# Optimization experiments

Hardware: AMD Instinct MI355X
Metric: run time of the kernel (lower is better)

## Reference

```python
import jax, jax.numpy as jnp
import numpy as np

# PGA G(3,0,1), basis order [1, e0,e1,e2,e3, e01,e02,e03,e12,e13,e23, e012,e013,e023,e123, e0123].
# Non-degenerate blades (no e0 factor) kept by the inner-product mask:
INNER_COORDS = jnp.array([0, 2, 3, 4, 8, 9, 10, 14])

B, S, C_IN, MV = 4, 2048, 3, 16
HID, NH, BLADES = 32, 8, 9


def setup_inputs() -> dict:
    key = jax.random.key(0)
    ks = jax.random.split(key, 8)
    return {
        "x": jax.random.normal(ks[0], (B, S, C_IN, MV), dtype=jnp.float32),
        "blade": jax.random.normal(ks[1], (BLADES, MV, MV), dtype=jnp.float32) * 0.3,
        "w_enter": jax.random.uniform(ks[2], (HID, C_IN, BLADES), dtype=jnp.float32),
        "w_q": jax.random.uniform(ks[3], (HID * NH, HID, BLADES), dtype=jnp.float32),
        "w_k": jax.random.uniform(ks[4], (HID, HID, BLADES), dtype=jnp.float32),
        "w_v": jax.random.uniform(ks[5], (HID, HID, BLADES), dtype=jnp.float32),
        "w_out": jax.random.uniform(ks[6], (HID, HID * NH, BLADES), dtype=jnp.float32),
        "w_final": jax.random.uniform(ks[7], (HID, HID, BLADES), dtype=jnp.float32),
    }


def equi_linear(w, blade, x):
    # torch: einsum('j i b, b x y, ... i x -> ... j y'); fuse blade into weight first.
    wb = jnp.einsum("jib,bxy->jixy", w, blade)  # [out, in, 16, 16]
    return jnp.einsum("jixy,bsix->bsjy", wb, x)


def equi_norm(x):
    ip = jnp.sum(jnp.take(x, INNER_COORDS, axis=-1) ** 2, axis=-1, keepdims=True)
    sq = jnp.mean(ip, axis=-2, keepdims=True)  # mean over mv channels
    return x / jnp.sqrt(sq)


def geometric_attention(hn, blade, w_q, w_k, w_v, w_out):
    b, s = hn.shape[0], hn.shape[1]
    q = equi_linear(w_q, blade, hn)  # [b, s, HID*NH, 16]
    k = equi_linear(w_k, blade, hn)  # [b, s, HID, 16]
    v = equi_linear(w_v, blade, hn)
    # rearrange '... items (hidden n_heads) mv -> ... n_heads items hidden mv'
    q = q.reshape(b, s, HID, NH, MV).transpose(0, 3, 1, 2, 4)  # [b, nh, s, HID, 16]
    qs = jnp.take(q, INNER_COORDS, axis=-1).reshape(b, NH, s, HID * 8)
    ks = jnp.take(k, INNER_COORDS, axis=-1).reshape(b, s, HID * 8)  # shared head (dim 1)
    vs = v.reshape(b, s, HID * MV)
    scale = 1.0 / jnp.sqrt(jnp.asarray(HID * 8, dtype=qs.dtype))
    scores = jnp.einsum("bhsd,btd->bhst", qs, ks) * scale  # [b, nh, s, s]
    attn = jax.nn.softmax(scores, axis=-1)
    out = jnp.einsum("bhst,btd->bhsd", attn, vs)  # [b, nh, s, HID*16]
    out = out[..., : HID * MV].reshape(b, NH, s, HID, MV)
    # '... heads items hidden x -> ... items (heads hidden) x'
    out = out.transpose(0, 2, 1, 3, 4).reshape(b, s, NH * HID, MV)
    return equi_linear(w_out, blade, out)  # [b, s, HID, 16]


def reference(x, blade, w_enter, w_q, w_k, w_v, w_out, w_final):
    h = equi_linear(w_enter, blade, x)  # initial projection -> [b, s, HID, 16]
    res = h
    hn = equi_norm(h)  # attention_equinorm
    a = geometric_attention(hn, blade, w_q, w_k, w_v, w_out)
    h = res + a  # residual around attention block
    return equi_linear(w_final, blade, h)  # final output projection
```

## Files before the change

kernel.cpp:

```cpp
#include <hip/hip_runtime.h>


typedef unsigned short u16;
typedef unsigned int u32;
typedef __attribute__((ext_vector_type(4))) float f32x4;
typedef __attribute__((ext_vector_type(8))) _Float16 half8;

__device__ inline u16 f2h(float f) {
  _Float16 h = (_Float16)f;
  return __builtin_bit_cast(u16, h);
}
__device__ inline float h2f(u16 u) { return (float)__builtin_bit_cast(_Float16, u); }

__device__ inline void async_cp16(const void* g, void* l) {
  __builtin_amdgcn_global_load_lds((const __attribute__((address_space(1))) u32*)g,
                                   (__attribute__((address_space(3))) u32*)l, 16, 0, 0);
}

__device__ inline f32x4 mfma16(half8 a, half8 b, f32x4 c) {
  return __builtin_amdgcn_mfma_f32_16x16x32_f16(a, b, c, 0, 0, 0);
}

template <int CTRL>
__device__ inline float dpp_mv(float v) {
  int i = __builtin_bit_cast(int, v);
  return __builtin_bit_cast(float, __builtin_amdgcn_update_dpp(i, i, CTRL, 0xf, 0xf, false));
}

#define IC_PACK 0xEA984320u

#define Q_LD 4096

__global__ void build_wb_enter(const float* __restrict__ we, const float* __restrict__ blade,
                               float* __restrict__ out) {
  int idx = blockIdx.x * 256 + threadIdx.x;
  if (idx >= 32 * 48 * 16) return;
  int j = idx / 768;
  int rem = idx - j * 768;
  int ix = rem >> 4, y = rem & 15;
  int i = ix >> 4, x = ix & 15;
  float acc = 0.f;
#pragma unroll
  for (int bb = 0; bb < 9; ++bb) acc += we[j * 27 + i * 9 + bb] * blade[bb * 256 + x * 16 + y];
  out[idx] = acc;
}

__global__ void build_wqkvT(const float* __restrict__ wq, const float* __restrict__ wk,
                            const float* __restrict__ wv, const float* __restrict__ blade,
                            u16* __restrict__ out) {
  int idx = blockIdx.x * 256 + threadIdx.x;
  if (idx >= 2816 * 1024) return;
  int k = idx & 1023, n = idx >> 10;
  int kk = k & 511;
  int i = kk >> 4, x = kk & 15;
  const float* w;
  int y;
  float scale = 1.0f;
  if (n < 2048) {
    int j = n >> 3;
    y = (IC_PACK >> ((n & 7) * 4)) & 15;
    w = wq + j * 288 + i * 9;
    scale = 0.09016844005556021f;
  } else if (n < 2304) {
    int m = n - 2048;
    int j = m >> 3;
    y = (IC_PACK >> ((m & 7) * 4)) & 15;
    w = wk + j * 288 + i * 9;
  } else {
    int m = n - 2304;
    int j = m >> 4;
    y = m & 15;
    w = wv + j * 288 + i * 9;
  }
  float acc = 0.f;
#pragma unroll
  for (int bb = 0; bb < 9; ++bb) acc += w[bb] * blade[bb * 256 + x * 16 + y];
  out[idx] = f2h(acc * scale);
}

__global__ void build_woutT(const float* __restrict__ wo, const float* __restrict__ blade,
                            u16* __restrict__ out) {
  int idx = blockIdx.x * 256 + threadIdx.x;
  if (idx >= 512 * 4096) return;
  int k = idx & 4095, n = idx >> 12;
  int j = n >> 4, y = n & 15;
  int c = k >> 4, x = k & 15;
  float acc = 0.f;
#pragma unroll
  for (int bb = 0; bb < 9; ++bb) acc += wo[j * 2304 + c * 9 + bb] * blade[bb * 256 + x * 16 + y];
  out[idx] = f2h(acc);
}

__global__ void build_wfinalT(const float* __restrict__ wf, const float* __restrict__ blade,
                              u16* __restrict__ out) {
  int idx = blockIdx.x * 256 + threadIdx.x;
  if (idx >= 512 * 512) return;
  int k = idx & 511, n = idx >> 9;
  int j = n >> 4, y = n & 15;
  int i = k >> 4, x = k & 15;
  float acc = 0.f;
#pragma unroll
  for (int bb = 0; bb < 9; ++bb) acc += wf[j * 288 + i * 9 + bb] * blade[bb * 256 + x * 16 + y];
  out[idx] = f2h(acc);
}

__global__ __launch_bounds__(256) void enter_norm(const float* __restrict__ x,
                                                  const float* __restrict__ wb,
                                                  float* __restrict__ h, u16* __restrict__ hn) {
  const int tid = threadIdx.x;
  const int tl = tid >> 5, j = tid & 31;
  const int token = blockIdx.x * 8 + tl;
  const float* xp = x + (size_t)token * 48;
  float xv[48];
#pragma unroll
  for (int q = 0; q < 12; ++q) {
    float4 t = ((const float4*)xp)[q];
    xv[q * 4 + 0] = t.x;
    xv[q * 4 + 1] = t.y;
    xv[q * 4 + 2] = t.z;
    xv[q * 4 + 3] = t.w;
  }
  float acc[16] = {};
  const float* wp = wb + j * 768;
#pragma unroll
  for (int t = 0; t < 48; ++t) {
    const float xs = xv[t];
    const float4* w4 = (const float4*)(wp + t * 16);
#pragma unroll
    for (int u = 0; u < 4; ++u) {
      float4 wv = w4[u];
      acc[u * 4 + 0] += xs * wv.x;
      acc[u * 4 + 1] += xs * wv.y;
      acc[u * 4 + 2] += xs * wv.z;
      acc[u * 4 + 3] += xs * wv.w;
    }
  }
  float ip = acc[0] * acc[0] + acc[2] * acc[2] + acc[3] * acc[3] + acc[4] * acc[4] +
             acc[8] * acc[8] + acc[9] * acc[9] + acc[10] * acc[10] + acc[14] * acc[14];
#pragma unroll
  for (int d = 1; d < 32; d <<= 1) ip += __shfl_xor(ip, d, 64);
  const float r = 1.0f / sqrtf(ip * (1.0f / 32.0f));
  float* hp = h + (size_t)token * 512 + j * 16;
#pragma unroll
  for (int u = 0; u < 4; ++u)
    ((float4*)hp)[u] = make_float4(acc[u * 4 + 0], acc[u * 4 + 1], acc[u * 4 + 2], acc[u * 4 + 3]);
  u16 hb[16], lb[16];
#pragma unroll
  for (int y = 0; y < 16; ++y) {
    float sv = acc[y] * r;
    u16 hv = f2h(sv);
    hb[y] = hv;
    lb[y] = f2h(sv - h2f(hv));
  }
  u16* hq = hn + (size_t)token * 1024 + j * 16;
  ((uint4*)hq)[0] = *(const uint4*)&hb[0];
  ((uint4*)hq)[1] = *(const uint4*)&hb[8];
  u16* lq = hq + 512;
  ((uint4*)lq)[0] = *(const uint4*)&lb[0];
  ((uint4*)lq)[1] = *(const uint4*)&lb[8];
}

template <int MODE>
__global__ __launch_bounds__(256) void gemm_bt(const u16* __restrict__ A,
                                               const u16* __restrict__ BT, int M, int N, int K,
                                               u16* __restrict__ Co, float* __restrict__ Cf,
                                               const float* __restrict__ res,
                                               u16* __restrict__ kvp, int ldc) {
  __shared__ u16 ltA[4096];
  __shared__ u16 ltB[4096];
  const int tid = threadIdx.x;
  const int lane = tid & 63;
  const int wid = tid >> 6;
  const int quad = lane >> 4, colc = lane & 15;
  const int m0 = blockIdx.y * 128, n0 = blockIdx.x * 128;
  const int wrow = (wid >> 1) * 64, wcol = (wid & 1) * 64;
  f32x4 acc[4][4] = {};
  const int r0 = tid >> 2;
  const int swk = (((tid & 3) ^ ((tid >> 2) & 3)) << 3);
  const u16* Ab = A + (size_t)(m0 + r0) * K + swk;
  const u16* Ab2 = Ab + (size_t)64 * K;
  const u16* Bb = BT + (size_t)(n0 + r0) * K + swk;
  const u16* Bb2 = Bb + (size_t)64 * K;
  const int swr = ((colc & 3) << 3);
  for (int k0 = 0; k0 < K; k0 += 32) {
    __syncthreads();
    async_cp16(Ab + k0, &ltA[tid * 8]);
    async_cp16(Ab2 + k0, &ltA[2048 + tid * 8]);
    async_cp16(Bb + k0, &ltB[tid * 8]);
    async_cp16(Bb2 + k0, &ltB[2048 + tid * 8]);
    __syncthreads();
    half8 af[4], bfr[4];
#pragma unroll
    for (int i2 = 0; i2 < 4; ++i2)
      af[i2] = *(const half8*)&ltA[(wrow + i2 * 16 + colc) * 32 + ((quad << 3) ^ swr)];
#pragma unroll
    for (int j2 = 0; j2 < 4; ++j2)
      bfr[j2] = *(const half8*)&ltB[(wcol + j2 * 16 + colc) * 32 + ((quad << 3) ^ swr)];
#pragma unroll
    for (int i2 = 0; i2 < 4; ++i2)
#pragma unroll
      for (int j2 = 0; j2 < 4; ++j2) acc[i2][j2] = mfma16(af[i2], bfr[j2], acc[i2][j2]);
  }
#pragma unroll
  for (int i2 = 0; i2 < 4; ++i2) {
#pragma unroll
    for (int j2 = 0; j2 < 4; ++j2) {
      const int mb = m0 + wrow + i2 * 16 + quad * 4;
      const int n = n0 + wcol + j2 * 16 + colc;
#pragma unroll
      for (int rg = 0; rg < 4; ++rg) {
        const int m = mb + rg;
        float v = acc[i2][j2][rg];
        if constexpr (MODE == 0) {
          u16 hv = f2h(v);
          if (n < 2048) {
            Co[(size_t)m * ldc + n] = hv;
            Co[(size_t)m * ldc + 2048 + n] = f2h(v - h2f(hv));
          } else {
            int bb = m >> 11, s = m & 2047, t = s >> 5, key = s & 31;
            size_t blk = ((size_t)(bb * 64 + t)) << 15;
            if (n < 2304) {
              int d = n - 2048;
              int off = key * 256 + ((((d >> 3) ^ (key & 7)) << 3)) + (d & 7);
              kvp[blk + off] = hv;
              kvp[blk + 8192 + off] = f2h(v - h2f(hv));
            } else {
              int vd = n - 2304;
              kvp[blk + 16384 + vd * 32 + ((((key >> 3) ^ (vd & 3)) << 3)) + (key & 7)] = hv;
            }
          }
        } else if constexpr (MODE == 1) {
          v += res[(size_t)m * ldc + n];
          Co[(size_t)m * ldc + n] = f2h(v * (1.0f / 256.0f));
        } else {
          Cf[(size_t)m * ldc + n] = v * 256.0f;
        }
      }
    }
  }
}

__global__ __launch_bounds__(256, 2) void flash_attn(const u16* __restrict__ qbuf,
                                                     const u16* __restrict__ kvp,
                                                     u16* __restrict__ out) {
  __shared__ u16 lds[32768];
  u16* kp = lds;
  u16* lp = lds + 8192;
  u16* vp = lds + 16384;
  u16* pbuf = lds + 8192;
  float* alpha_s = (float*)(lds + 8192 + 2560);
  float* l_s = (float*)(lds + 8192 + 2560 + 128);
  const int tid = threadIdx.x, lane = tid & 63, wid = tid >> 6;
  const int quad = lane >> 4, colc = lane & 15;
  const int b = blockIdx.z, h = blockIdx.y, qb = blockIdx.x;
  half8 qh[8], ql[8];
  {
    const u16* qr = qbuf + (size_t)(b * 2048 + qb * 64 + wid * 16 + colc) * Q_LD + h * 8;
#pragma unroll
    for (int kb = 0; kb < 8; ++kb) {
      qh[kb] = *(const half8*)(qr + (kb * 4 + quad) * 64);
      ql[kb] = *(const half8*)(qr + 2048 + (kb * 4 + quad) * 64);
    }
  }
  f32x4 oacc[4][8] = {};
  float mrun[4], lrun[4];
#pragma unroll
  for (int rg = 0; rg < 4; ++rg) {
    mrun[rg] = -1e30f;
    lrun[rg] = 0.f;
  }
  const u16* kvb = kvp + ((size_t)(b * 64) << 15);
  const int x0 = colc & 7;
  for (int it = 0; it < 64; ++it) {
    __syncthreads();
    {
      const u16* src = kvb + ((size_t)it << 15);
#pragma unroll
      for (int c = 0; c < 16; ++c) {
        int e = c * 256 + tid;
        async_cp16(src + e * 8, &lds[e * 8]);
      }
    }
    __syncthreads();
    f32x4 s0a = {}, s0b = {}, s1a = {}, s1b = {};
#pragma unroll
    for (int kb = 0; kb < 8; ++kb) {
      const int sw = (((kb * 4 + quad) ^ x0) << 3);
      half8 khi0 = *(const half8*)&kp[colc * 256 + sw];
      half8 khi1 = *(const half8*)&kp[(16 + colc) * 256 + sw];
      half8 klo0 = *(const half8*)&lp[colc * 256 + sw];
      half8 klo1 = *(const half8*)&lp[(16 + colc) * 256 + sw];
      s0a = mfma16(qh[kb], khi0, s0a);
      s0b = mfma16(ql[kb], khi0, s0b);
      s1a = mfma16(qh[kb], khi1, s1a);
      s1b = mfma16(ql[kb], khi1, s1b);
      if (kb & 1) {
        s0b = mfma16(qh[kb], klo0, s0b);
        s1b = mfma16(qh[kb], klo1, s1b);
      } else {
        s0a = mfma16(qh[kb], klo0, s0a);
        s1a = mfma16(qh[kb], klo1, s1a);
      }
    }
    f32x4 sfr[2];
    sfr[0] = s0a + s0b;
    sfr[1] = s1a + s1b;
    float mx[4];
#pragma unroll
    for (int rg = 0; rg < 4; ++rg) mx[rg] = fmaxf(sfr[0][rg], sfr[1][rg]);
#pragma unroll
    for (int rg = 0; rg < 4; ++rg) mx[rg] = fmaxf(mx[rg], dpp_mv<0x121>(mx[rg]));
#pragma unroll
    for (int rg = 0; rg < 4; ++rg) mx[rg] = fmaxf(mx[rg], dpp_mv<0x122>(mx[rg]));
#pragma unroll
    for (int rg = 0; rg < 4; ++rg) mx[rg] = fmaxf(mx[rg], dpp_mv<0x124>(mx[rg]));
#pragma unroll
    for (int rg = 0; rg < 4; ++rg) mx[rg] = fmaxf(mx[rg], dpp_mv<0x128>(mx[rg]));
    float al[4], pv0[4], pv1[4], rs[4];
#pragma unroll
    for (int rg = 0; rg < 4; ++rg) {
      float mn = fmaxf(mrun[rg], mx[rg]);
      al[rg] = exp2f(mrun[rg] - mn);
      mrun[rg] = mn;
      pv0[rg] = exp2f(sfr[0][rg] - mn);
      pv1[rg] = exp2f(sfr[1][rg] - mn);
      rs[rg] = pv0[rg] + pv1[rg];
    }
#pragma unroll
    for (int rg = 0; rg < 4; ++rg) rs[rg] += dpp_mv<0x121>(rs[rg]);
#pragma unroll
    for (int rg = 0; rg < 4; ++rg) rs[rg] += dpp_mv<0x122>(rs[rg]);
#pragma unroll
    for (int rg = 0; rg < 4; ++rg) rs[rg] += dpp_mv<0x124>(rs[rg]);
#pragma unroll
    for (int rg = 0; rg < 4; ++rg) rs[rg] += dpp_mv<0x128>(rs[rg]);
    __syncthreads();
    const int prow = wid * 16 + quad * 4;
#pragma unroll
    for (int rg = 0; rg < 4; ++rg) {
      lrun[rg] = lrun[rg] * al[rg] + rs[rg];
      pbuf[(prow + rg) * 40 + colc] = f2h(pv0[rg]);
      pbuf[(prow + rg) * 40 + 16 + colc] = f2h(pv1[rg]);
    }
    if (colc == 0) {
#pragma unroll
      for (int rg = 0; rg < 4; ++rg) alpha_s[prow + rg] = al[rg];
    }
    __syncthreads();
    half8 vf[8];
#pragma unroll
    for (int vb = 0; vb < 8; ++vb) {
      const int vd = wid * 128 + vb * 16 + colc;
      vf[vb] = *(const half8*)&vp[vd * 32 + ((quad ^ (vd & 3)) << 3)];
    }
    half8 pf[4];
#pragma unroll
    for (int pa = 0; pa < 4; ++pa)
      pf[pa] = *(const half8*)&pbuf[(pa * 16 + colc) * 40 + quad * 8];
    float av[4][4];
#pragma unroll
    for (int pa = 0; pa < 4; ++pa)
#pragma unroll
      for (int rg = 0; rg < 4; ++rg) av[pa][rg] = alpha_s[pa * 16 + quad * 4 + rg];
#pragma unroll
    for (int pa = 0; pa < 4; ++pa)
#pragma unroll
      for (int vb = 0; vb < 8; ++vb)
#pragma unroll
        for (int rg = 0; rg < 4; ++rg) oacc[pa][vb][rg] *= av[pa][rg];
#pragma unroll
    for (int vb = 0; vb < 8; ++vb)
#pragma unroll
      for (int pa = 0; pa < 4; ++pa) oacc[pa][vb] = mfma16(pf[pa], vf[vb], oacc[pa][vb]);
  }
  {
    const int prow = wid * 16 + quad * 4;
    if (colc == 0) {
#pragma unroll
      for (int rg = 0; rg < 4; ++rg) l_s[prow + rg] = lrun[rg];
    }
  }
  __syncthreads();
  u16* ob = out + ((size_t)b * 2048 + qb * 64) * 4096 + h * 512 + wid * 128;
#pragma unroll
  for (int pa = 0; pa < 4; ++pa) {
    float li[4];
#pragma unroll
    for (int rg = 0; rg < 4; ++rg) li[rg] = 1.0f / l_s[pa * 16 + quad * 4 + rg];
#pragma unroll
    for (int vb = 0; vb < 8; ++vb)
#pragma unroll
      for (int rg = 0; rg < 4; ++rg)
        ob[(size_t)(pa * 16 + quad * 4 + rg) * 4096 + vb * 16 + colc] =
            f2h(oacc[pa][vb][rg] * li[rg]);
  }
}

extern "C" void kernel_launch(void* const* d_in, const int* in_sizes, int n_in, void* d_out,
                              int out_size, void* d_ws, size_t ws_size, hipStream_t stream) {
  const float* x = (const float*)d_in[0];
  const float* blade = (const float*)d_in[1];
  const float* w_enter = (const float*)d_in[2];
  const float* w_q = (const float*)d_in[3];
  const float* w_k = (const float*)d_in[4];
  const float* w_v = (const float*)d_in[5];
  const float* w_out = (const float*)d_in[6];
  const float* w_final = (const float*)d_in[7];
  float* out = (float*)d_out;

  char* ws = (char*)d_ws;
  size_t off = 0;
  auto alloc = [&](size_t bytes) {
    void* p = ws + off;
    off = (off + bytes + 255) & ~(size_t)255;
    return p;
  };
  float* wb_enter = (float*)alloc((size_t)32 * 48 * 16 * 4);
  u16* wqkvT = (u16*)alloc((size_t)2816 * 1024 * 2);
  u16* woutT = (u16*)alloc((size_t)512 * 4096 * 2);
  u16* wfinT = (u16*)alloc((size_t)512 * 512 * 2);
  float* hbuf = (float*)alloc((size_t)8192 * 512 * 4);
  u16* hn2 = (u16*)alloc((size_t)8192 * 1024 * 2);
  u16* qbuf = (u16*)alloc((size_t)8192 * Q_LD * 2);
  u16* kvp = (u16*)alloc((size_t)4 * 64 * 32768 * 2);
  u16* attno = (u16*)alloc((size_t)8192 * 4096 * 2);
  u16* h2 = (u16*)alloc((size_t)8192 * 512 * 2);

  build_wb_enter<<<96, 256, 0, stream>>>(w_enter, blade, wb_enter);
  build_wqkvT<<<11264, 256, 0, stream>>>(w_q, w_k, w_v, blade, wqkvT);
  build_woutT<<<8192, 256, 0, stream>>>(w_out, blade, woutT);
  build_wfinalT<<<1024, 256, 0, stream>>>(w_final, blade, wfinT);
  enter_norm<<<1024, 256, 0, stream>>>(x, wb_enter, hbuf, hn2);
  gemm_bt<0><<<dim3(22, 64), 256, 0, stream>>>(hn2, wqkvT, 8192, 2816, 1024, qbuf, nullptr,
                                               nullptr, kvp, Q_LD);
  flash_attn<<<dim3(32, 8, 4), 256, 0, stream>>>(qbuf, kvp, attno);
  gemm_bt<1><<<dim3(4, 64), 256, 0, stream>>>(attno, woutT, 8192, 512, 4096, h2, nullptr, hbuf,
                                              nullptr, 512);
  gemm_bt<2><<<dim3(4, 64), 256, 0, stream>>>(h2, wfinT, 8192, 512, 512, nullptr, out, nullptr,
                                              nullptr, 512);
}
```

Before: 954.7 us.

## Skip unchanged-max rescale, vectorize V stores, give P buffer its own LDS

Moves the P/alpha scratch buffers out of the K-low region into dedicated shared memory, which removes one block barrier per key tile. Adds a per-wave flag so the output-accumulator rescale is skipped when no row's running max changed. Changes the V swizzle so the GEMM epilogue can write four consecutive keys with one 8-byte store instead of four scalar stores. The trade-offs are slightly more LDS per block, which may affect occupancy, and an extra flag reduction with a wave vote.

```diff
diff --git a/kernel.cpp b/kernel.cpp
--- a/kernel.cpp
+++ b/kernel.cpp
@@ -207,33 +207,51 @@
     for (int j2 = 0; j2 < 4; ++j2) {
       const int mb = m0 + wrow + i2 * 16 + quad * 4;
       const int n = n0 + wcol + j2 * 16 + colc;
-#pragma unroll
-      for (int rg = 0; rg < 4; ++rg) {
-        const int m = mb + rg;
-        float v = acc[i2][j2][rg];
-        if constexpr (MODE == 0) {
-          u16 hv = f2h(v);
-          if (n < 2048) {
+      if constexpr (MODE == 0) {
+        if (n < 2048) {
+#pragma unroll
+          for (int rg = 0; rg < 4; ++rg) {
+            const int m = mb + rg;
+            float v = acc[i2][j2][rg];
+            u16 hv = f2h(v);
             Co[(size_t)m * ldc + n] = hv;
             Co[(size_t)m * ldc + 2048 + n] = f2h(v - h2f(hv));
+          }
+        } else if (n < 2304) {
+          const int d = n - 2048;
+#pragma unroll
+          for (int rg = 0; rg < 4; ++rg) {
+            const int m = mb + rg;
+            int bb2 = m >> 11, s = m & 2047, t = s >> 5, key = s & 31;
+            size_t blk = ((size_t)(bb2 * 64 + t)) << 15;
+            int off2 = key * 256 + ((((d >> 3) ^ (key & 7)) << 3)) + (d & 7);
+            float v = acc[i2][j2][rg];
+            u16 hv = f2h(v);
+            kvp[blk + off2] = hv;
+            kvp[blk + 8192 + off2] = f2h(v - h2f(hv));
+          }
+        } else {
+          const int vd = n - 2304;
+          int bb2 = mb >> 11, s0 = mb & 2047, t = s0 >> 5, key0 = s0 & 31;
+          size_t blk = ((size_t)(bb2 * 64 + t)) << 15;
+          u16 tmp[4];
+#pragma unroll
+          for (int rg = 0; rg < 4; ++rg) tmp[rg] = f2h(acc[i2][j2][rg]);
+          size_t idx =
+              blk + 16384 + vd * 32 + ((((key0 >> 3) ^ ((vd >> 1) & 3)) << 3)) + (key0 & 7);
+          *(uint2*)&kvp[idx] = *(const uint2*)tmp;
+        }
+      } else {
+#pragma unroll
+        for (int rg = 0; rg < 4; ++rg) {
+          const int m = mb + rg;
+          float v = acc[i2][j2][rg];
+          if constexpr (MODE == 1) {
+            v += res[(size_t)m * ldc + n];
+            Co[(size_t)m * ldc + n] = f2h(v * (1.0f / 256.0f));
           } else {
-            int bb = m >> 11, s = m & 2047, t = s >> 5, key = s & 31;
-            size_t blk = ((size_t)(bb * 64 + t)) << 15;
-            if (n < 2304) {
-              int d = n - 2048;
-              int off = key * 256 + ((((d >> 3) ^ (key & 7)) << 3)) + (d & 7);
-              kvp[blk + off] = hv;
-              kvp[blk + 8192 + off] = f2h(v - h2f(hv));
-            } else {
-              int vd = n - 2304;
-              kvp[blk + 16384 + vd * 32 + ((((key >> 3) ^ (vd & 3)) << 3)) + (key & 7)] = hv;
-            }
+            Cf[(size_t)m * ldc + n] = v * 256.0f;
           }
-        } else if constexpr (MODE == 1) {
-          v += res[(size_t)m * ldc + n];
-          Co[(size_t)m * ldc + n] = f2h(v * (1.0f / 256.0f));
-        } else {
-          Cf[(size_t)m * ldc + n] = v * 256.0f;
         }
       }
     }
@@ -243,13 +261,14 @@
 __global__ __launch_bounds__(256, 2) void flash_attn(const u16* __restrict__ qbuf,
                                                      const u16* __restrict__ kvp,
                                                      u16* __restrict__ out) {
-  __shared__ u16 lds[32768];
+  __shared__ u16 lds[35600];
   u16* kp = lds;
   u16* lp = lds + 8192;
   u16* vp = lds + 16384;
-  u16* pbuf = lds + 8192;
-  float* alpha_s = (float*)(lds + 8192 + 2560);
-  float* l_s = (float*)(lds + 8192 + 2560 + 128);
+  u16* pbuf = lds + 32768;
+  float* alpha_s = (float*)(lds + 35328);
+  float* l_s = (float*)(lds + 35456);
+  int* flg = (int*)(lds + 35584);
   const int tid = threadIdx.x, lane = tid & 63, wid = tid >> 6;
   const int quad = lane >> 4, colc = lane & 15;
   const int b = blockIdx.z, h = blockIdx.y, qb = blockIdx.x;
@@ -334,7 +353,6 @@
     for (int rg = 0; rg < 4; ++rg) rs[rg] += dpp_mv<0x124>(rs[rg]);
 #pragma unroll
     for (int rg = 0; rg < 4; ++rg) rs[rg] += dpp_mv<0x128>(rs[rg]);
-    __syncthreads();
     const int prow = wid * 16 + quad * 4;
 #pragma unroll
     for (int rg = 0; rg < 4; ++rg) {
@@ -342,6 +360,12 @@
       pbuf[(prow + rg) * 40 + colc] = f2h(pv0[rg]);
       pbuf[(prow + rg) * 40 + 16 + colc] = f2h(pv1[rg]);
     }
+    {
+      float nd = __builtin_fabsf(al[0] - 1.f) + __builtin_fabsf(al[1] - 1.f) +
+                 __builtin_fabsf(al[2] - 1.f) + __builtin_fabsf(al[3] - 1.f);
+      int own = __any(nd != 0.f);
+      if (lane == 0) flg[wid] = own;
+    }
     if (colc == 0) {
 #pragma unroll
       for (int rg = 0; rg < 4; ++rg) alpha_s[prow + rg] = al[rg];
@@ -351,23 +375,25 @@
 #pragma unroll
     for (int vb = 0; vb < 8; ++vb) {
       const int vd = wid * 128 + vb * 16 + colc;
-      vf[vb] = *(const half8*)&vp[vd * 32 + ((quad ^ (vd & 3)) << 3)];
+      vf[vb] = *(const half8*)&vp[vd * 32 + ((quad ^ ((vd >> 1) & 3)) << 3)];
     }
     half8 pf[4];
 #pragma unroll
-    for (int pa = 0; pa < 4; ++pa)
-      pf[pa] = *(const half8*)&pbuf[(pa * 16 + colc) * 40 + quad * 8];
-    float av[4][4];
-#pragma unroll
-    for (int pa = 0; pa < 4; ++pa)
-#pragma unroll
-      for (int rg = 0; rg < 4; ++rg) av[pa][rg] = alpha_s[pa * 16 + quad * 4 + rg];
-#pragma unroll
-    for (int pa = 0; pa < 4; ++pa)
-#pragma unroll
-      for (int vb = 0; vb < 8; ++vb)
-#pragma unroll
-        for (int rg = 0; rg < 4; ++rg) oacc[pa][vb][rg] *= av[pa][rg];
+    for (int pa = 0; pa < 4; ++pa) pf[pa] = *(const half8*)&pbuf[(pa * 16 + colc) * 40 + quad * 8];
+    const int need = flg[0] | flg[1] | flg[2] | flg[3];
+    if (need) {
+      float av[4][4];
+#pragma unroll
+      for (int pa = 0; pa < 4; ++pa)
+#pragma unroll
+        for (int rg = 0; rg < 4; ++rg) av[pa][rg] = alpha_s[pa * 16 + quad * 4 + rg];
+#pragma unroll
+      for (int pa = 0; pa < 4; ++pa)
+#pragma unroll
+        for (int vb = 0; vb < 8; ++vb)
+#pragma unroll
+          for (int rg = 0; rg < 4; ++rg) oacc[pa][vb][rg] *= av[pa][rg];
+    }
 #pragma unroll
     for (int vb = 0; vb < 8; ++vb)
 #pragma unroll
```

After: 984.4 us. +3.1%, slower.
